# Performance work log

Measured on AMD Instinct MI355X. Metric: run time of the kernel, lower is better.

The kernel has to match this reference:

```python
import jax, jax.numpy as jnp
import numpy as np

N_USERS = 100_000
N_ENTITIES = 400_000
N_NODES = N_USERS + N_ENTITIES  # 500k
DIM = 64
N_EDGES = 2_000_000
BATCH = 4096
N_LAYERS = 3
CF_WEIGHT = 1.0
L2_REG = 1e-4


def setup_inputs() -> dict:
    key = jax.random.key(0)
    k_emb, k_e, k_u, k_p, k_n = jax.random.split(key, 5)
    # xavier_uniform on (N, D): bound = sqrt(6/(N+D))
    bound = float(np.sqrt(6.0 / (N_NODES + DIM)))
    emb = jax.random.uniform(k_emb, (N_NODES, DIM), jnp.float32, -bound, bound)
    edge_index = jax.random.randint(k_e, (2, N_EDGES), 0, N_NODES, dtype=jnp.int32)
    user_idx = jax.random.randint(k_u, (BATCH,), 0, N_USERS, dtype=jnp.int32)
    pos_item = jax.random.randint(k_p, (BATCH,), 0, N_NODES, dtype=jnp.int32)
    neg_item = jax.random.randint(k_n, (BATCH,), 0, N_NODES, dtype=jnp.int32)
    return {"emb": emb, "edge_index": edge_index, "user_idx": user_idx,
            "pos_item": pos_item, "neg_item": neg_item}


def _lightgcn(emb, edge_index, n_layers):
    # LGConv(normalize=True): x' = D^{-1/2} A D^{-1/2} x, no self loops.
    n = emb.shape[0]
    src, dst = edge_index[0], edge_index[1]
    deg = jax.ops.segment_sum(jnp.ones_like(dst, dtype=emb.dtype), dst,
                              num_segments=n)
    dinv = jnp.where(deg > 0, jax.lax.rsqrt(jnp.maximum(deg, 1e-12)), 0.0)
    norm = dinv[src] * dinv[dst]  # [E]
    x = emb
    acc = emb  # layer-0 term of the mean over stacked layers
    for _ in range(n_layers):
        msgs = x[src] * norm[:, None]  # [E, D] gather + scale
        x = jax.ops.segment_sum(msgs, dst, num_segments=n)  # scatter-add
        acc = acc + x
    return acc / (n_layers + 1)  # mean over (layers+1) stacked embeddings


def reference(emb, edge_index, user_idx, pos_item, neg_item):
    all_layer = _lightgcn(emb, edge_index, N_LAYERS)
    u = all_layer[user_idx]
    p = all_layer[pos_item]
    n_ = all_layer[neg_item]
    pos_score = jnp.sum(u * p, axis=-1)
    neg_score = jnp.sum(u * n_, axis=-1)
    # BPRLoss: -mean(logsigmoid(pos - neg)) == mean(softplus(neg - pos))
    cf_loss = jnp.mean(jax.nn.softplus(neg_score - pos_score))
    u_ego = emb[user_idx]
    p_ego = emb[pos_item]
    n_ego = emb[neg_item]
    reg_loss = 0.5 * (jnp.sum(u_ego ** 2) + jnp.sum(p_ego ** 2)
                      + jnp.sum(n_ego ** 2)) / float(BATCH)
    return CF_WEIGHT * cf_loss + L2_REG * reg_loss
```

## Files before the change

kernel.cpp:

```cpp
#include <hip/hip_runtime.h>
#include <cstdint>
#include <cstddef>

#define N_USERS   100000
#define N_NODES   500000
#define DIM       64
#define N_EDGES   2000000
#define BATCH     4096
#define SCAN_B    1024
#define NBLK      ((N_NODES + SCAN_B - 1) / SCAN_B)
#define X1C_CAP   280000
#define LA_CAP    100000
#define EDG4_BLK  ((N_EDGES / 4 + 255) / 256)
#define PROP_BLK  2048

#define RANGES    31
#define RANGE_SZ  16384
#define RANGE_TOT (RANGES * RANGE_SZ)
#define HSLICES   32
#define HIST_BLK  (RANGES * HSLICES)
#define ESLICE    (N_EDGES / HSLICES)
#define EINT4     (ESLICE / 4)
#define DEG4_BLK  ((N_NODES / 4 + 255) / 256)

#define NSPECIAL  (EDG4_BLK + DEG4_BLK)
#define ECD_TOTAL (NSPECIAL * 14)

typedef unsigned char uchar;
typedef unsigned short ushort;
typedef unsigned int uint;

__device__ __forceinline__ ushort f2bf(float f) {
    uint u = __float_as_uint(f);
    uint r = u + 0x7FFFu + ((u >> 16) & 1u);
    return (ushort)(r >> 16);
}
__device__ __forceinline__ float bflo(uint u) { return __uint_as_float(u << 16); }
__device__ __forceinline__ float bfhi(uint u) { return __uint_as_float(u & 0xFFFF0000u); }

__global__ void k_mark(const int* __restrict__ u, const int* __restrict__ p,
                       const int* __restrict__ n, uchar* __restrict__ f3,
                       uchar* __restrict__ fA, uchar* __restrict__ fB) {
    int i = blockIdx.x * blockDim.x + threadIdx.x;
    if (i >= 3 * BATCH) return;
    int idx;
    if (i < BATCH)          idx = u[i];
    else if (i < 2 * BATCH) idx = p[i - BATCH];
    else                    idx = n[i - 2 * BATCH];
    f3[idx] = 1; fA[idx] = 1; fB[idx] = 1;
}

__global__ void k_histexp(const int* __restrict__ src, const int* __restrict__ dst,
                          uchar* __restrict__ degp8, const uchar* __restrict__ f3,
                          uchar* __restrict__ fA) {
    __shared__ uint cnt[RANGE_SZ / 4];
    if (blockIdx.x < HIST_BLK) {
        int s = blockIdx.x / RANGES;
        int r = blockIdx.x - s * RANGES;
        for (int k = threadIdx.x; k < RANGE_SZ / 4; k += 256) cnt[k] = 0;
        __syncthreads();
        int base = r * RANGE_SZ;
        const int4* d4 = (const int4*)(dst + s * ESLICE);
        for (int t = threadIdx.x; t < EINT4; t += 256) {
            int4 d = d4[t];
            uint l;
            l = (uint)(d.x - base); if (l < RANGE_SZ) atomicAdd(&cnt[l >> 2], 1u << ((l & 3) << 3));
            l = (uint)(d.y - base); if (l < RANGE_SZ) atomicAdd(&cnt[l >> 2], 1u << ((l & 3) << 3));
            l = (uint)(d.z - base); if (l < RANGE_SZ) atomicAdd(&cnt[l >> 2], 1u << ((l & 3) << 3));
            l = (uint)(d.w - base); if (l < RANGE_SZ) atomicAdd(&cnt[l >> 2], 1u << ((l & 3) << 3));
        }
        __syncthreads();
        uint* out = (uint*)(degp8 + (size_t)s * RANGE_TOT) + r * (RANGE_SZ / 4);
        for (int k = threadIdx.x; k < RANGE_SZ / 4; k += 256) out[k] = cnt[k];
    } else {
        int t = (blockIdx.x - HIST_BLK) * blockDim.x + threadIdx.x;
        if (t < N_EDGES / 4) {
            int4 s0 = ((const int4*)src)[t];
            int4 d0 = ((const int4*)dst)[t];
            if (f3[d0.x] && !fA[s0.x]) fA[s0.x] = 1;
            if (f3[d0.y] && !fA[s0.y]) fA[s0.y] = 1;
            if (f3[d0.z] && !fA[s0.z]) fA[s0.z] = 1;
            if (f3[d0.w] && !fA[s0.w]) fA[s0.w] = 1;
        }
    }
}

__global__ void k_expconvdeg(const int* __restrict__ src, const int* __restrict__ dst,
                             const uchar* __restrict__ fA, uchar* __restrict__ fB,
                             const uchar* __restrict__ degp8, int* __restrict__ degsum,
                             const float* __restrict__ emb, ushort* __restrict__ embs) {
    uint b = blockIdx.x;
    uint g = b / 14u;
    uint r = b - g * 14u;
    if (r == 0u) {
        if (g < EDG4_BLK) {
            int t = (int)g * 256 + threadIdx.x;
            if (t < N_EDGES / 4) {
                int4 s0 = ((const int4*)src)[t];
                int4 d0 = ((const int4*)dst)[t];
                if (fA[d0.x] && !fB[s0.x]) fB[s0.x] = 1;
                if (fA[d0.y] && !fB[s0.y]) fB[s0.y] = 1;
                if (fA[d0.z] && !fB[s0.z]) fB[s0.z] = 1;
                if (fA[d0.w] && !fB[s0.w]) fB[s0.w] = 1;
            }
        } else {
            int j = (int)(g - EDG4_BLK) * 256 + threadIdx.x;
            if (j < N_NODES / 4) {
                int j4 = j * 4;
                int d0 = 0, d1 = 0, d2 = 0, d3 = 0;
                #pragma unroll
                for (int s = 0; s < HSLICES; ++s) {
                    uchar4 c = *(const uchar4*)(degp8 + (size_t)s * RANGE_TOT + j4);
                    d0 += c.x; d1 += c.y; d2 += c.z; d3 += c.w;
                }
                ((int4*)degsum)[j] = make_int4(d0, d1, d2, d3);
            }
        }
    } else {
        int c = (int)(g * 13u + r - 1u) * 256 + threadIdx.x;
        if (c < N_NODES * 16) {
            float4 v = ((const float4*)emb)[c];
            uint2 o;
            o.x = (uint)f2bf(v.x) | ((uint)f2bf(v.y) << 16);
            o.y = (uint)f2bf(v.z) | ((uint)f2bf(v.w) << 16);
            ((uint2*)embs)[c] = o;
        }
    }
}

__global__ void k_scanA(const int* __restrict__ degsum, const uchar* __restrict__ fA,
                        const uchar* __restrict__ fB, int* __restrict__ bsumD,
                        int* __restrict__ bsumP) {
    __shared__ int sD[SCAN_B];
    __shared__ int sP[SCAN_B];
    int i = blockIdx.x * SCAN_B + threadIdx.x;
    int d = 0, pk = 0;
    if (i < N_NODES) { d = degsum[i]; pk = (int)fA[i] | ((int)fB[i] << 16); }
    sD[threadIdx.x] = d; sP[threadIdx.x] = pk;
    __syncthreads();
    for (int off = SCAN_B / 2; off; off >>= 1) {
        if (threadIdx.x < off) {
            sD[threadIdx.x] += sD[threadIdx.x + off];
            sP[threadIdx.x] += sP[threadIdx.x + off];
        }
        __syncthreads();
    }
    if (threadIdx.x == 0) { bsumD[blockIdx.x] = sD[0]; bsumP[blockIdx.x] = sP[0]; }
}

__global__ void k_scanB(const int* __restrict__ bsumD, const int* __restrict__ bsumP,
                        int* __restrict__ boffD, int* __restrict__ boffA,
                        int* __restrict__ boffB, int* __restrict__ counts) {
    __shared__ int sD[512];
    __shared__ int sA[512];
    __shared__ int sB[512];
    int d = (threadIdx.x < NBLK) ? bsumD[threadIdx.x] : 0;
    int p = (threadIdx.x < NBLK) ? bsumP[threadIdx.x] : 0;
    int a = p & 0xFFFF, b = p >> 16;
    sD[threadIdx.x] = d; sA[threadIdx.x] = a; sB[threadIdx.x] = b;
    __syncthreads();
    for (int off = 1; off < 512; off <<= 1) {
        int tD = (threadIdx.x >= off) ? sD[threadIdx.x - off] : 0;
        int tA = (threadIdx.x >= off) ? sA[threadIdx.x - off] : 0;
        int tB = (threadIdx.x >= off) ? sB[threadIdx.x - off] : 0;
        __syncthreads();
        sD[threadIdx.x] += tD; sA[threadIdx.x] += tA; sB[threadIdx.x] += tB;
        __syncthreads();
    }
    if (threadIdx.x < NBLK) {
        boffD[threadIdx.x] = sD[threadIdx.x] - d;
        boffA[threadIdx.x] = sA[threadIdx.x] - a;
        boffB[threadIdx.x] = sB[threadIdx.x] - b;
    }
    if (threadIdx.x == 511) { counts[0] = sA[511]; counts[1] = sB[511]; }
}

__global__ void k_scanC(const int* __restrict__ degsum, const uchar* __restrict__ fA,
                        const uchar* __restrict__ fB,
                        const int* __restrict__ boffD, const int* __restrict__ boffA,
                        const int* __restrict__ boffB,
                        int* __restrict__ rowstart, float* __restrict__ dinv,
                        int* __restrict__ mapA, int* __restrict__ mapB,
                        int4* __restrict__ listA4, int4* __restrict__ listB4) {
    __shared__ int sD[SCAN_B];
    __shared__ int sP[SCAN_B];
    int i = blockIdx.x * SCAN_B + threadIdx.x;
    int d = 0, a = 0, b = 0;
    if (i < N_NODES) { d = degsum[i]; a = (int)fA[i]; b = (int)fB[i]; }
    sD[threadIdx.x] = d; sP[threadIdx.x] = a | (b << 16);
    __syncthreads();
    for (int off = 1; off < SCAN_B; off <<= 1) {
        int tD = (threadIdx.x >= off) ? sD[threadIdx.x - off] : 0;
        int tP = (threadIdx.x >= off) ? sP[threadIdx.x - off] : 0;
        __syncthreads();
        sD[threadIdx.x] += tD; sP[threadIdx.x] += tP;
        __syncthreads();
    }
    if (i < N_NODES) {
        int exD = sD[threadIdx.x] - d + boffD[blockIdx.x];
        int incP = sP[threadIdx.x];
        int exA = (incP & 0xFFFF) - a + boffA[blockIdx.x];
        int exB = (incP >> 16) - b + boffB[blockIdx.x];
        rowstart[i] = exD;
        float dv = (d > 0) ? rsqrtf((float)d) : 0.0f;
        dinv[i] = dv;
        mapA[i] = a ? exA : -1;
        mapB[i] = b ? exB : -1;
        int4 ent = make_int4(exD, exD + d, __float_as_int(dv), 0);
        if (a) listA4[exA] = ent;
        if (b) listB4[exB] = ent;
    }
}

__global__ void k_scatter(const int* __restrict__ src, const int* __restrict__ dst,
                          const uchar* __restrict__ fB, int* __restrict__ rowstart,
                          int* __restrict__ csr_src) {
    int t = blockIdx.x * blockDim.x + threadIdx.x;
    if (t < N_EDGES / 4) {
        int4 s0 = ((const int4*)src)[t];
        int4 d0 = ((const int4*)dst)[t];
        if (fB[d0.x]) csr_src[atomicAdd(&rowstart[d0.x], 1)] = s0.x;
        if (fB[d0.y]) csr_src[atomicAdd(&rowstart[d0.y], 1)] = s0.y;
        if (fB[d0.z]) csr_src[atomicAdd(&rowstart[d0.z], 1)] = s0.z;
        if (fB[d0.w]) csr_src[atomicAdd(&rowstart[d0.w], 1)] = s0.w;
    }
}

__global__ void k_prop1(const ushort* __restrict__ embs, const int4* __restrict__ listB4,
                        const int* __restrict__ counts, const int* __restrict__ csr_src,
                        const float* __restrict__ dinv, ushort* __restrict__ x1c) {
    int lane = threadIdx.x & 63;
    int sub = lane >> 4, q = lane & 15;
    int wv = (blockIdx.x * blockDim.x + threadIdx.x) >> 6;
    int nw = (gridDim.x * blockDim.x) >> 6;
    int cnt = counts[1];
    for (; wv < cnt; wv += nw) {
        int4 nb = listB4[wv];
        float4 acc = {0.f, 0.f, 0.f, 0.f};
        for (int i = nb.x + sub; i < nb.y; i += 4) {
            int s = csr_src[i];
            float dvs = dinv[s];
            uint2 u = *(const uint2*)(embs + (size_t)s * DIM + q * 4);
            acc.x = fmaf(bflo(u.x), dvs, acc.x);
            acc.y = fmaf(bfhi(u.x), dvs, acc.y);
            acc.z = fmaf(bflo(u.y), dvs, acc.z);
            acc.w = fmaf(bfhi(u.y), dvs, acc.w);
        }
        for (int off = 16; off <= 32; off <<= 1) {
            acc.x += __shfl_xor(acc.x, off, 64);
            acc.y += __shfl_xor(acc.y, off, 64);
            acc.z += __shfl_xor(acc.z, off, 64);
            acc.w += __shfl_xor(acc.w, off, 64);
        }
        if (sub == 0) {
            float dv = __int_as_float(nb.z);
            float d2 = dv * dv;
            uint2 o;
            o.x = (uint)f2bf(acc.x * d2) | ((uint)f2bf(acc.y * d2) << 16);
            o.y = (uint)f2bf(acc.z * d2) | ((uint)f2bf(acc.w * d2) << 16);
            *(uint2*)(x1c + (size_t)wv * DIM + q * 4) = o;
        }
    }
}

__global__ void k_prop2(const ushort* __restrict__ x1c, const int* __restrict__ mapB,
                        const int4* __restrict__ listA4, const int* __restrict__ counts,
                        const int* __restrict__ csr_src, ushort* __restrict__ x2c) {
    int lane = threadIdx.x & 63;
    int sub = lane >> 4, q = lane & 15;
    int wv = (blockIdx.x * blockDim.x + threadIdx.x) >> 6;
    int nw = (gridDim.x * blockDim.x) >> 6;
    int cnt = counts[0];
    for (; wv < cnt; wv += nw) {
        int4 nb = listA4[wv];
        float4 acc = {0.f, 0.f, 0.f, 0.f};
        for (int i = nb.x + sub; i < nb.y; i += 4) {
            int s = csr_src[i];
            int slot = mapB[s];
            uint2 u = *(const uint2*)(x1c + (size_t)slot * DIM + q * 4);
            acc.x += bflo(u.x); acc.y += bfhi(u.x);
            acc.z += bflo(u.y); acc.w += bfhi(u.y);
        }
        for (int off = 16; off <= 32; off <<= 1) {
            acc.x += __shfl_xor(acc.x, off, 64);
            acc.y += __shfl_xor(acc.y, off, 64);
            acc.z += __shfl_xor(acc.z, off, 64);
            acc.w += __shfl_xor(acc.w, off, 64);
        }
        if (sub == 0) {
            float dv = __int_as_float(nb.z);
            float d2 = dv * dv;
            uint2 o;
            o.x = (uint)f2bf(acc.x * d2) | ((uint)f2bf(acc.y * d2) << 16);
            o.y = (uint)f2bf(acc.z * d2) | ((uint)f2bf(acc.w * d2) << 16);
            *(uint2*)(x2c + (size_t)wv * DIM + q * 4) = o;
        }
    }
}

__device__ __forceinline__ float x3_row(const ushort* __restrict__ x2c,
                                        const int* __restrict__ mapA,
                                        const int* __restrict__ csr_src,
                                        const int4* __restrict__ listB4,
                                        const int* __restrict__ mapB,
                                        int t, int lane) {
    int4 nb = listB4[mapB[t]];
    float acc = 0.f;
    for (int i = nb.x; i < nb.y; ++i) {
        int s = csr_src[i];
        int slot = mapA[s];
        acc += __uint_as_float((uint)x2c[(size_t)slot * DIM + lane] << 16);
    }
    return acc * __int_as_float(nb.z);
}

__global__ void k_loss(const float* __restrict__ emb, const ushort* __restrict__ x1c,
                       const ushort* __restrict__ x2c,
                       const int* __restrict__ mapA, const int* __restrict__ mapB,
                       const int4* __restrict__ listB4, const int* __restrict__ csr_src,
                       const float* __restrict__ dinv,
                       const int* __restrict__ u, const int* __restrict__ p,
                       const int* __restrict__ n, float* __restrict__ out) {
    int lane = threadIdx.x & 63;
    int w = (blockIdx.x * blockDim.x + threadIdx.x) >> 6;
    if (w >= BATCH) return;
    int ui = u[w], pi = p[w], ni = n[w];
    float dvu = dinv[ui], dvp = dinv[pi], dvn = dinv[ni];
    float rdu = dvu > 0.f ? 1.f / dvu : 0.f;
    float rdp = dvp > 0.f ? 1.f / dvp : 0.f;
    float rdn = dvn > 0.f ? 1.f / dvn : 0.f;
    float ue = emb[(size_t)ui * DIM + lane];
    float pe = emb[(size_t)pi * DIM + lane];
    float ne = emb[(size_t)ni * DIM + lane];
    float u1 = __uint_as_float((uint)x1c[(size_t)mapB[ui] * DIM + lane] << 16) * rdu;
    float p1 = __uint_as_float((uint)x1c[(size_t)mapB[pi] * DIM + lane] << 16) * rdp;
    float n1 = __uint_as_float((uint)x1c[(size_t)mapB[ni] * DIM + lane] << 16) * rdn;
    float u2 = __uint_as_float((uint)x2c[(size_t)mapA[ui] * DIM + lane] << 16) * rdu;
    float p2 = __uint_as_float((uint)x2c[(size_t)mapA[pi] * DIM + lane] << 16) * rdp;
    float n2 = __uint_as_float((uint)x2c[(size_t)mapA[ni] * DIM + lane] << 16) * rdn;
    float u3 = x3_row(x2c, mapA, csr_src, listB4, mapB, ui, lane);
    float p3 = x3_row(x2c, mapA, csr_src, listB4, mapB, pi, lane);
    float n3 = x3_row(x2c, mapA, csr_src, listB4, mapB, ni, lane);
    float uall = 0.25f * (ue + u1 + u2 + u3);
    float pall = 0.25f * (pe + p1 + p2 + p3);
    float nall = 0.25f * (ne + n1 + n2 + n3);
    float pos = uall * pall;
    float neg = uall * nall;
    float sq  = ue * ue + pe * pe + ne * ne;
    for (int off = 32; off; off >>= 1) {
        pos += __shfl_xor(pos, off, 64);
        neg += __shfl_xor(neg, off, 64);
        sq  += __shfl_xor(sq,  off, 64);
    }
    if (lane == 0) {
        float z = neg - pos;
        float sp = fmaxf(z, 0.0f) + log1pf(expf(-fabsf(z)));
        float contrib = sp * (1.0f / BATCH) + 1e-4f * 0.5f * sq * (1.0f / BATCH);
        atomicAdd(out, contrib);
    }
}

extern "C" void kernel_launch(void* const* d_in, const int* in_sizes, int n_in,
                              void* d_out, int out_size, void* d_ws, size_t ws_size,
                              hipStream_t stream) {
    const float* emb  = (const float*)d_in[0];
    const int*   edge = (const int*)d_in[1];
    const int*   src  = edge;
    const int*   dst  = edge + N_EDGES;
    const int*   uidx = (const int*)d_in[2];
    const int*   pidx = (const int*)d_in[3];
    const int*   nidx = (const int*)d_in[4];
    float* out = (float*)d_out;

    char* w = (char*)d_ws;
    ushort* embs    = (ushort*)w;                w += (size_t)N_NODES * DIM * 2;
    ushort* x1c     = (ushort*)w;                w += (size_t)X1C_CAP * DIM * 2;
    ushort* x2c     = (ushort*)w;                w += (size_t)LA_CAP * DIM * 2;
    float*  dinv    = (float*)w;                 w += (size_t)N_NODES * 4;
    int*    rowstart= (int*)w;                   w += (size_t)N_NODES * 4;
    int*    csr_src = (int*)w;                   w += (size_t)N_EDGES * 4;
    int*    mapA    = (int*)w;                   w += (size_t)N_NODES * 4;
    int*    mapB    = (int*)w;                   w += (size_t)N_NODES * 4;
    int*    degsum  = (int*)w;                   w += (size_t)N_NODES * 4;
    int4*   listA4  = (int4*)w;                  w += (size_t)LA_CAP * 16;
    int4*   listB4  = (int4*)w;                  w += (size_t)X1C_CAP * 16;
    uchar*  degp8   = (uchar*)w;                 w += (size_t)HSLICES * RANGE_TOT;
    char*   zbase   = w;
    uchar*  flags   = (uchar*)w;                 w += (size_t)3 * N_NODES;
    uchar*  f3 = flags;
    uchar*  fA = flags + N_NODES;
    uchar*  fB = flags + 2 * N_NODES;
    size_t  zbytes  = (size_t)(w - zbase);
    int*    bsumD   = (int*)w;                   w += (size_t)NBLK * 4;
    int*    boffD   = (int*)w;                   w += (size_t)NBLK * 4;
    int*    bsumP   = (int*)w;                   w += (size_t)NBLK * 4;
    int*    boffA   = (int*)w;                   w += (size_t)NBLK * 4;
    int*    boffB   = (int*)w;                   w += (size_t)NBLK * 4;
    int*    counts  = (int*)w;                   w += 16;

    hipMemsetAsync(zbase, 0, zbytes, stream);
    hipMemsetAsync(out, 0, 4, stream);

    k_mark<<<(3 * BATCH + 255) / 256, 256, 0, stream>>>(uidx, pidx, nidx, f3, fA, fB);

    k_histexp<<<HIST_BLK + EDG4_BLK, 256, 0, stream>>>(src, dst, degp8, f3, fA);

    k_expconvdeg<<<ECD_TOTAL, 256, 0, stream>>>(src, dst, fA, fB, degp8, degsum,
                                                emb, embs);

    k_scanA<<<NBLK, SCAN_B, 0, stream>>>(degsum, fA, fB, bsumD, bsumP);
    k_scanB<<<1, 512, 0, stream>>>(bsumD, bsumP, boffD, boffA, boffB, counts);
    k_scanC<<<NBLK, SCAN_B, 0, stream>>>(degsum, fA, fB, boffD, boffA, boffB,
                                         rowstart, dinv, mapA, mapB, listA4, listB4);

    k_scatter<<<EDG4_BLK, 256, 0, stream>>>(src, dst, fB, rowstart, csr_src);

    k_prop1<<<PROP_BLK, 256, 0, stream>>>(embs, listB4, counts, csr_src, dinv, x1c);
    k_prop2<<<PROP_BLK, 256, 0, stream>>>(x1c, mapB, listA4, counts, csr_src, x2c);

    k_loss<<<(BATCH * 64 + 255) / 256, 256, 0, stream>>>(
        emb, x1c, x2c, mapA, mapB, listB4, csr_src, dinv, uidx, pidx, nidx, out);
}
```

Measured before the change: 449.1 us.

## Pack frontier flags into bitmaps, fold degree sum into scan, widen prop loads

Replaces the three per-node byte flag arrays with 32-bit-word bitmaps set via atomicOr, which cuts the random-access footprint of the frontier expansion and scatter passes. The per-slice degree reduction moves from the expansion kernel into scanA, which now reads the byte histograms directly, so the expansion kernel only expands and converts embeddings. The propagation kernels switch to 16-byte loads with 8 lanes per row and 8 rows in flight, using eight accumulators. Risks include atomic contention on shared bitmap words, byte-wise strided reads in scanA, and a longer shuffle reduction.

```diff
diff --git a/kernel.cpp b/kernel.cpp
--- a/kernel.cpp
+++ b/kernel.cpp
@@ -13,6 +13,7 @@
 #define LA_CAP    100000
 #define EDG4_BLK  ((N_EDGES / 4 + 255) / 256)
 #define PROP_BLK  2048
+#define NBMW      (N_NODES / 32)
 
 #define RANGES    31
 #define RANGE_SZ  16384
@@ -21,10 +22,8 @@
 #define HIST_BLK  (RANGES * HSLICES)
 #define ESLICE    (N_EDGES / HSLICES)
 #define EINT4     (ESLICE / 4)
-#define DEG4_BLK  ((N_NODES / 4 + 255) / 256)
-
-#define NSPECIAL  (EDG4_BLK + DEG4_BLK)
-#define ECD_TOTAL (NSPECIAL * 14)
+
+#define EC_TOTAL  (EDG4_BLK * 17)
 
 typedef unsigned char uchar;
 typedef unsigned short ushort;
@@ -38,21 +37,33 @@
 __device__ __forceinline__ float bflo(uint u) { return __uint_as_float(u << 16); }
 __device__ __forceinline__ float bfhi(uint u) { return __uint_as_float(u & 0xFFFF0000u); }
 
+__device__ __forceinline__ int getbit(const uint* __restrict__ bm, int i) {
+    return (bm[i >> 5] >> (i & 31)) & 1;
+}
+__device__ __forceinline__ void setbit_dedup(uint* __restrict__ bm, int i) {
+    uint m = 1u << (i & 31);
+    uint* p = &bm[i >> 5];
+    if (!(*p & m)) atomicOr(p, m);
+}
+
 __global__ void k_mark(const int* __restrict__ u, const int* __restrict__ p,
-                       const int* __restrict__ n, uchar* __restrict__ f3,
-                       uchar* __restrict__ fA, uchar* __restrict__ fB) {
+                       const int* __restrict__ n, uint* __restrict__ f3w,
+                       uint* __restrict__ fAw, uint* __restrict__ fBw) {
     int i = blockIdx.x * blockDim.x + threadIdx.x;
     if (i >= 3 * BATCH) return;
     int idx;
     if (i < BATCH)          idx = u[i];
     else if (i < 2 * BATCH) idx = p[i - BATCH];
     else                    idx = n[i - 2 * BATCH];
-    f3[idx] = 1; fA[idx] = 1; fB[idx] = 1;
+    uint m = 1u << (idx & 31);
+    atomicOr(&f3w[idx >> 5], m);
+    atomicOr(&fAw[idx >> 5], m);
+    atomicOr(&fBw[idx >> 5], m);
 }
 
 __global__ void k_histexp(const int* __restrict__ src, const int* __restrict__ dst,
-                          uchar* __restrict__ degp8, const uchar* __restrict__ f3,
-                          uchar* __restrict__ fA) {
+                          uchar* __restrict__ degp8, const uint* __restrict__ f3w,
+                          uint* __restrict__ fAw) {
     __shared__ uint cnt[RANGE_SZ / 4];
     if (blockIdx.x < HIST_BLK) {
         int s = blockIdx.x / RANGES;
@@ -77,47 +88,32 @@
         if (t < N_EDGES / 4) {
             int4 s0 = ((const int4*)src)[t];
             int4 d0 = ((const int4*)dst)[t];
-            if (f3[d0.x] && !fA[s0.x]) fA[s0.x] = 1;
-            if (f3[d0.y] && !fA[s0.y]) fA[s0.y] = 1;
-            if (f3[d0.z] && !fA[s0.z]) fA[s0.z] = 1;
-            if (f3[d0.w] && !fA[s0.w]) fA[s0.w] = 1;
-        }
-    }
-}
-
-__global__ void k_expconvdeg(const int* __restrict__ src, const int* __restrict__ dst,
-                             const uchar* __restrict__ fA, uchar* __restrict__ fB,
-                             const uchar* __restrict__ degp8, int* __restrict__ degsum,
-                             const float* __restrict__ emb, ushort* __restrict__ embs) {
+            if (getbit(f3w, d0.x)) setbit_dedup(fAw, s0.x);
+            if (getbit(f3w, d0.y)) setbit_dedup(fAw, s0.y);
+            if (getbit(f3w, d0.z)) setbit_dedup(fAw, s0.z);
+            if (getbit(f3w, d0.w)) setbit_dedup(fAw, s0.w);
+        }
+    }
+}
+
+__global__ void k_expconv(const int* __restrict__ src, const int* __restrict__ dst,
+                          const uint* __restrict__ fAw, uint* __restrict__ fBw,
+                          const float* __restrict__ emb, ushort* __restrict__ embs) {
     uint b = blockIdx.x;
-    uint g = b / 14u;
-    uint r = b - g * 14u;
+    uint g = b / 17u;
+    uint r = b - g * 17u;
     if (r == 0u) {
-        if (g < EDG4_BLK) {
-            int t = (int)g * 256 + threadIdx.x;
-            if (t < N_EDGES / 4) {
-                int4 s0 = ((const int4*)src)[t];
-                int4 d0 = ((const int4*)dst)[t];
-                if (fA[d0.x] && !fB[s0.x]) fB[s0.x] = 1;
-                if (fA[d0.y] && !fB[s0.y]) fB[s0.y] = 1;
-                if (fA[d0.z] && !fB[s0.z]) fB[s0.z] = 1;
-                if (fA[d0.w] && !fB[s0.w]) fB[s0.w] = 1;
-            }
-        } else {
-            int j = (int)(g - EDG4_BLK) * 256 + threadIdx.x;
-            if (j < N_NODES / 4) {
-                int j4 = j * 4;
-                int d0 = 0, d1 = 0, d2 = 0, d3 = 0;
-                #pragma unroll
-                for (int s = 0; s < HSLICES; ++s) {
-                    uchar4 c = *(const uchar4*)(degp8 + (size_t)s * RANGE_TOT + j4);
-                    d0 += c.x; d1 += c.y; d2 += c.z; d3 += c.w;
-                }
-                ((int4*)degsum)[j] = make_int4(d0, d1, d2, d3);
-            }
+        int t = (int)g * 256 + threadIdx.x;
+        if (t < N_EDGES / 4) {
+            int4 s0 = ((const int4*)src)[t];
+            int4 d0 = ((const int4*)dst)[t];
+            if (getbit(fAw, d0.x)) setbit_dedup(fBw, s0.x);
+            if (getbit(fAw, d0.y)) setbit_dedup(fBw, s0.y);
+            if (getbit(fAw, d0.z)) setbit_dedup(fBw, s0.z);
+            if (getbit(fAw, d0.w)) setbit_dedup(fBw, s0.w);
         }
     } else {
-        int c = (int)(g * 13u + r - 1u) * 256 + threadIdx.x;
+        int c = (int)(g * 16u + r - 1u) * 256 + threadIdx.x;
         if (c < N_NODES * 16) {
             float4 v = ((const float4*)emb)[c];
             uint2 o;
@@ -128,14 +124,19 @@
     }
 }
 
-__global__ void k_scanA(const int* __restrict__ degsum, const uchar* __restrict__ fA,
-                        const uchar* __restrict__ fB, int* __restrict__ bsumD,
-                        int* __restrict__ bsumP) {
+__global__ void k_scanA(const uchar* __restrict__ degp8, const uint* __restrict__ fAw,
+                        const uint* __restrict__ fBw, int* __restrict__ degsum,
+                        int* __restrict__ bsumD, int* __restrict__ bsumP) {
     __shared__ int sD[SCAN_B];
     __shared__ int sP[SCAN_B];
     int i = blockIdx.x * SCAN_B + threadIdx.x;
     int d = 0, pk = 0;
-    if (i < N_NODES) { d = degsum[i]; pk = (int)fA[i] | ((int)fB[i] << 16); }
+    if (i < N_NODES) {
+        #pragma unroll
+        for (int s = 0; s < HSLICES; ++s) d += (int)degp8[(size_t)s * RANGE_TOT + i];
+        degsum[i] = d;
+        pk = getbit(fAw, i) | (getbit(fBw, i) << 16);
+    }
     sD[threadIdx.x] = d; sP[threadIdx.x] = pk;
     __syncthreads();
     for (int off = SCAN_B / 2; off; off >>= 1) {
@@ -175,8 +176,8 @@
     if (threadIdx.x == 511) { counts[0] = sA[511]; counts[1] = sB[511]; }
 }
 
-__global__ void k_scanC(const int* __restrict__ degsum, const uchar* __restrict__ fA,
-                        const uchar* __restrict__ fB,
+__global__ void k_scanC(const int* __restrict__ degsum, const uint* __restrict__ fAw,
+                        const uint* __restrict__ fBw,
                         const int* __restrict__ boffD, const int* __restrict__ boffA,
                         const int* __restrict__ boffB,
                         int* __restrict__ rowstart, float* __restrict__ dinv,
@@ -186,7 +187,11 @@
     __shared__ int sP[SCAN_B];
     int i = blockIdx.x * SCAN_B + threadIdx.x;
     int d = 0, a = 0, b = 0;
-    if (i < N_NODES) { d = degsum[i]; a = (int)fA[i]; b = (int)fB[i]; }
+    if (i < N_NODES) {
+        d = degsum[i];
+        a = getbit(fAw, i);
+        b = getbit(fBw, i);
+    }
     sD[threadIdx.x] = d; sP[threadIdx.x] = a | (b << 16);
     __syncthreads();
     for (int off = 1; off < SCAN_B; off <<= 1) {
@@ -213,16 +218,16 @@
 }
 
 __global__ void k_scatter(const int* __restrict__ src, const int* __restrict__ dst,
-                          const uchar* __restrict__ fB, int* __restrict__ rowstart,
+                          const uint* __restrict__ fBw, int* __restrict__ rowstart,
                           int* __restrict__ csr_src) {
     int t = blockIdx.x * blockDim.x + threadIdx.x;
     if (t < N_EDGES / 4) {
         int4 s0 = ((const int4*)src)[t];
         int4 d0 = ((const int4*)dst)[t];
-        if (fB[d0.x]) csr_src[atomicAdd(&rowstart[d0.x], 1)] = s0.x;
-        if (fB[d0.y]) csr_src[atomicAdd(&rowstart[d0.y], 1)] = s0.y;
-        if (fB[d0.z]) csr_src[atomicAdd(&rowstart[d0.z], 1)] = s0.z;
-        if (fB[d0.w]) csr_src[atomicAdd(&rowstart[d0.w], 1)] = s0.w;
+        if (getbit(fBw, d0.x)) csr_src[atomicAdd(&rowstart[d0.x], 1)] = s0.x;
+        if (getbit(fBw, d0.y)) csr_src[atomicAdd(&rowstart[d0.y], 1)] = s0.y;
+        if (getbit(fBw, d0.z)) csr_src[atomicAdd(&rowstart[d0.z], 1)] = s0.z;
+        if (getbit(fBw, d0.w)) csr_src[atomicAdd(&rowstart[d0.w], 1)] = s0.w;
     }
 }
 
@@ -230,35 +235,38 @@
                         const int* __restrict__ counts, const int* __restrict__ csr_src,
                         const float* __restrict__ dinv, ushort* __restrict__ x1c) {
     int lane = threadIdx.x & 63;
-    int sub = lane >> 4, q = lane & 15;
+    int sub = lane >> 3, q = lane & 7;
     int wv = (blockIdx.x * blockDim.x + threadIdx.x) >> 6;
     int nw = (gridDim.x * blockDim.x) >> 6;
     int cnt = counts[1];
     for (; wv < cnt; wv += nw) {
         int4 nb = listB4[wv];
-        float4 acc = {0.f, 0.f, 0.f, 0.f};
-        for (int i = nb.x + sub; i < nb.y; i += 4) {
+        float a0 = 0.f, a1 = 0.f, a2 = 0.f, a3 = 0.f;
+        float a4 = 0.f, a5 = 0.f, a6 = 0.f, a7 = 0.f;
+        for (int i = nb.x + sub; i < nb.y; i += 8) {
             int s = csr_src[i];
             float dvs = dinv[s];
-            uint2 u = *(const uint2*)(embs + (size_t)s * DIM + q * 4);
-            acc.x = fmaf(bflo(u.x), dvs, acc.x);
-            acc.y = fmaf(bfhi(u.x), dvs, acc.y);
-            acc.z = fmaf(bflo(u.y), dvs, acc.z);
-            acc.w = fmaf(bfhi(u.y), dvs, acc.w);
-        }
-        for (int off = 16; off <= 32; off <<= 1) {
-            acc.x += __shfl_xor(acc.x, off, 64);
-            acc.y += __shfl_xor(acc.y, off, 64);
-            acc.z += __shfl_xor(acc.z, off, 64);
-            acc.w += __shfl_xor(acc.w, off, 64);
+            uint4 u = *(const uint4*)(embs + (size_t)s * DIM + q * 8);
+            a0 = fmaf(bflo(u.x), dvs, a0); a1 = fmaf(bfhi(u.x), dvs, a1);
+            a2 = fmaf(bflo(u.y), dvs, a2); a3 = fmaf(bfhi(u.y), dvs, a3);
+            a4 = fmaf(bflo(u.z), dvs, a4); a5 = fmaf(bfhi(u.z), dvs, a5);
+            a6 = fmaf(bflo(u.w), dvs, a6); a7 = fmaf(bfhi(u.w), dvs, a7);
+        }
+        for (int off = 8; off <= 32; off <<= 1) {
+            a0 += __shfl_xor(a0, off, 64); a1 += __shfl_xor(a1, off, 64);
+            a2 += __shfl_xor(a2, off, 64); a3 += __shfl_xor(a3, off, 64);
+            a4 += __shfl_xor(a4, off, 64); a5 += __shfl_xor(a5, off, 64);
+            a6 += __shfl_xor(a6, off, 64); a7 += __shfl_xor(a7, off, 64);
         }
         if (sub == 0) {
             float dv = __int_as_float(nb.z);
             float d2 = dv * dv;
-            uint2 o;
-            o.x = (uint)f2bf(acc.x * d2) | ((uint)f2bf(acc.y * d2) << 16);
-            o.y = (uint)f2bf(acc.z * d2) | ((uint)f2bf(acc.w * d2) << 16);
-            *(uint2*)(x1c + (size_t)wv * DIM + q * 4) = o;
+            uint4 o;
+            o.x = (uint)f2bf(a0 * d2) | ((uint)f2bf(a1 * d2) << 16);
+            o.y = (uint)f2bf(a2 * d2) | ((uint)f2bf(a3 * d2) << 16);
+            o.z = (uint)f2bf(a4 * d2) | ((uint)f2bf(a5 * d2) << 16);
+            o.w = (uint)f2bf(a6 * d2) | ((uint)f2bf(a7 * d2) << 16);
+            *(uint4*)(x1c + (size_t)wv * DIM + q * 8) = o;
         }
     }
 }
@@ -267,33 +275,38 @@
                         const int4* __restrict__ listA4, const int* __restrict__ counts,
                         const int* __restrict__ csr_src, ushort* __restrict__ x2c) {
     int lane = threadIdx.x & 63;
-    int sub = lane >> 4, q = lane & 15;
+    int sub = lane >> 3, q = lane & 7;
     int wv = (blockIdx.x * blockDim.x + threadIdx.x) >> 6;
     int nw = (gridDim.x * blockDim.x) >> 6;
     int cnt = counts[0];
     for (; wv < cnt; wv += nw) {
         int4 nb = listA4[wv];
-        float4 acc = {0.f, 0.f, 0.f, 0.f};
-        for (int i = nb.x + sub; i < nb.y; i += 4) {
+        float a0 = 0.f, a1 = 0.f, a2 = 0.f, a3 = 0.f;
+        float a4 = 0.f, a5 = 0.f, a6 = 0.f, a7 = 0.f;
+        for (int i = nb.x + sub; i < nb.y; i += 8) {
             int s = csr_src[i];
             int slot = mapB[s];
-            uint2 u = *(const uint2*)(x1c + (size_t)slot * DIM + q * 4);
-            acc.x += bflo(u.x); acc.y += bfhi(u.x);
-            acc.z += bflo(u.y); acc.w += bfhi(u.y);
-        }
-        for (int off = 16; off <= 32; off <<= 1) {
-            acc.x += __shfl_xor(acc.x, off, 64);
-            acc.y += __shfl_xor(acc.y, off, 64);
-            acc.z += __shfl_xor(acc.z, off, 64);
-            acc.w += __shfl_xor(acc.w, off, 64);
+            uint4 u = *(const uint4*)(x1c + (size_t)slot * DIM + q * 8);
+            a0 += bflo(u.x); a1 += bfhi(u.x);
+            a2 += bflo(u.y); a3 += bfhi(u.y);
+            a4 += bflo(u.z); a5 += bfhi(u.z);
+            a6 += bflo(u.w); a7 += bfhi(u.w);
+        }
+        for (int off = 8; off <= 32; off <<= 1) {
+            a0 += __shfl_xor(a0, off, 64); a1 += __shfl_xor(a1, off, 64);
+            a2 += __shfl_xor(a2, off, 64); a3 += __shfl_xor(a3, off, 64);
+            a4 += __shfl_xor(a4, off, 64); a5 += __shfl_xor(a5, off, 64);
+            a6 += __shfl_xor(a6, off, 64); a7 += __shfl_xor(a7, off, 64);
         }
         if (sub == 0) {
             float dv = __int_as_float(nb.z);
             float d2 = dv * dv;
-            uint2 o;
-            o.x = (uint)f2bf(acc.x * d2) | ((uint)f2bf(acc.y * d2) << 16);
-            o.y = (uint)f2bf(acc.z * d2) | ((uint)f2bf(acc.w * d2) << 16);
-            *(uint2*)(x2c + (size_t)wv * DIM + q * 4) = o;
+            uint4 o;
+            o.x = (uint)f2bf(a0 * d2) | ((uint)f2bf(a1 * d2) << 16);
+            o.y = (uint)f2bf(a2 * d2) | ((uint)f2bf(a3 * d2) << 16);
+            o.z = (uint)f2bf(a4 * d2) | ((uint)f2bf(a5 * d2) << 16);
+            o.w = (uint)f2bf(a6 * d2) | ((uint)f2bf(a7 * d2) << 16);
+            *(uint4*)(x2c + (size_t)wv * DIM + q * 8) = o;
         }
     }
 }
@@ -386,10 +399,9 @@
     int4*   listB4  = (int4*)w;                  w += (size_t)X1C_CAP * 16;
     uchar*  degp8   = (uchar*)w;                 w += (size_t)HSLICES * RANGE_TOT;
     char*   zbase   = w;
-    uchar*  flags   = (uchar*)w;                 w += (size_t)3 * N_NODES;
-    uchar*  f3 = flags;
-    uchar*  fA = flags + N_NODES;
-    uchar*  fB = flags + 2 * N_NODES;
+    uint*   f3w     = (uint*)w;                  w += (size_t)NBMW * 4;
+    uint*   fAw     = (uint*)w;                  w += (size_t)NBMW * 4;
+    uint*   fBw     = (uint*)w;                  w += (size_t)NBMW * 4;
     size_t  zbytes  = (size_t)(w - zbase);
     int*    bsumD   = (int*)w;                   w += (size_t)NBLK * 4;
     int*    boffD   = (int*)w;                   w += (size_t)NBLK * 4;
@@ -401,19 +413,18 @@
     hipMemsetAsync(zbase, 0, zbytes, stream);
     hipMemsetAsync(out, 0, 4, stream);
 
-    k_mark<<<(3 * BATCH + 255) / 256, 256, 0, stream>>>(uidx, pidx, nidx, f3, fA, fB);
-
-    k_histexp<<<HIST_BLK + EDG4_BLK, 256, 0, stream>>>(src, dst, degp8, f3, fA);
-
-    k_expconvdeg<<<ECD_TOTAL, 256, 0, stream>>>(src, dst, fA, fB, degp8, degsum,
-                                                emb, embs);
-
-    k_scanA<<<NBLK, SCAN_B, 0, stream>>>(degsum, fA, fB, bsumD, bsumP);
+    k_mark<<<(3 * BATCH + 255) / 256, 256, 0, stream>>>(uidx, pidx, nidx, f3w, fAw, fBw);
+
+    k_histexp<<<HIST_BLK + EDG4_BLK, 256, 0, stream>>>(src, dst, degp8, f3w, fAw);
+
+    k_expconv<<<EC_TOTAL, 256, 0, stream>>>(src, dst, fAw, fBw, emb, embs);
+
+    k_scanA<<<NBLK, SCAN_B, 0, stream>>>(degp8, fAw, fBw, degsum, bsumD, bsumP);
     k_scanB<<<1, 512, 0, stream>>>(bsumD, bsumP, boffD, boffA, boffB, counts);
-    k_scanC<<<NBLK, SCAN_B, 0, stream>>>(degsum, fA, fB, boffD, boffA, boffB,
+    k_scanC<<<NBLK, SCAN_B, 0, stream>>>(degsum, fAw, fBw, boffD, boffA, boffB,
                                          rowstart, dinv, mapA, mapB, listA4, listB4);
 
-    k_scatter<<<EDG4_BLK, 256, 0, stream>>>(src, dst, fB, rowstart, csr_src);
+    k_scatter<<<EDG4_BLK, 256, 0, stream>>>(src, dst, fBw, rowstart, csr_src);
 
     k_prop1<<<PROP_BLK, 256, 0, stream>>>(embs, listB4, counts, csr_src, dinv, x1c);
     k_prop2<<<PROP_BLK, 256, 0, stream>>>(x1c, mapB, listA4, counts, csr_src, x2c);
```

Result: slower. 516.3 us (+15.0%).
